# Kernel optimization log

Hardware: AMD Instinct MI355X
Metric: run time of the kernel (lower is better)

## Reference

```python
import jax, jax.numpy as jnp
import numpy as np

SIZES = (20, 20, 20, 20, 20)          # formula_oh_sizes
OH_N = sum(SIZES)                      # 100
NUM_BINS = 65536                       # spect_bin.get_num_bins()
EPS_SIZE = 1e-4                        # eps added to subset size
IN_EPS = 1e-5                          # torch InstanceNorm1d default eps


def thermometer_oh(counts):
    # StructuredOneHot with accum=True: per-element thermometer encoding.
    # counts: (N, E) element counts -> (N, sum(SIZES)) with out[j]=1 iff j < count.
    outs = [(jnp.arange(s, dtype=counts.dtype)[None, :] < counts[:, i:i + 1]).astype(jnp.float32)
            for i, s in enumerate(SIZES)]
    return jnp.concatenate(outs, axis=-1)


def inorm(x):
    # InstanceNorm1d (affine=False) as applied here: normalize over last dim per row.
    m = jnp.mean(x, axis=-1, keepdims=True)
    v = jnp.var(x, axis=-1, keepdims=True)
    return (x - m) * jax.lax.rsqrt(v + IN_EPS)


def _lin(key, fan_in, fan_out):
    k1, k2 = jax.random.split(key)
    bound = 1.0 / np.sqrt(fan_in)
    W = jax.random.uniform(k1, (fan_in, fan_out), jnp.float32, -bound, bound)
    b = jax.random.uniform(k2, (fan_out,), jnp.float32, -bound, bound)
    return W, b


def setup_inputs():
    key = jax.random.key(0)
    ks = jax.random.split(key, 12)
    B, A, GF, S, P, E, D = 8, 48, 256, 4096, 32, 5, 256
    vert_feat_in = jax.random.normal(ks[0], (B, A, GF), jnp.float32)
    vert_mask_in = jnp.ones((B, A), jnp.float32)
    elem_idx = jax.random.randint(ks[1], (B, A), 0, E)
    vert_element_oh = jax.nn.one_hot(elem_idx, E, dtype=jnp.float32)
    adj_oh = jnp.zeros((B, A, A), jnp.float32)                      # unused by forward path
    atom_subsets = jax.random.randint(ks[2], (B, S, A), 0, 2).astype(jnp.int32)
    atom_subsets_peaks = jnp.zeros((1,), jnp.float32)               # unused (mass_idx/intensity used)
    mass_idx = jax.random.randint(ks[3], (B, S, P), 0, NUM_BINS).astype(jnp.int32)
    intensity = jax.random.uniform(ks[4], (B, S, P), jnp.float32)
    combine_W, combine_b = _lin(ks[5], OH_N + GF, GF)
    l1_W, l1_b = _lin(ks[6], GF, D)
    l2a_W, l2a_b = _lin(ks[7], D, D)
    l2b_W, l2b_b = _lin(ks[8], D, D)
    score_W, score_b = _lin(ks[9], D, 1)
    return {
        'vert_feat_in': vert_feat_in, 'vert_mask_in': vert_mask_in,
        'vert_element_oh': vert_element_oh, 'adj_oh': adj_oh,
        'atom_subsets': atom_subsets, 'atom_subsets_peaks': atom_subsets_peaks,
        'mass_idx': mass_idx, 'intensity': intensity,
        'combine_W': combine_W, 'combine_b': combine_b,
        'l1_W': l1_W, 'l1_b': l1_b, 'l2a_W': l2a_W, 'l2a_b': l2a_b,
        'l2b_W': l2b_W, 'l2b_b': l2b_b, 'score_W': score_W, 'score_b': score_b,
    }


def reference(vert_feat_in, vert_mask_in, vert_element_oh, adj_oh, atom_subsets,
              atom_subsets_peaks, mass_idx, intensity,
              combine_W, combine_b, l1_W, l1_b, l2a_W, l2a_b, l2b_W, l2b_b,
              score_W, score_b):
    B, A, GF = vert_feat_in.shape
    _, S, _ = atom_subsets.shape
    subsets_f = atom_subsets.astype(jnp.float32)
    masked_vert = vert_feat_in * vert_mask_in[:, :, None]               # (B,A,GF)
    subsets_masked = subsets_f * vert_mask_in[:, None, :]               # (B,S,A)
    # weighted sum of vertex features over each subset
    sws = jnp.einsum('bag,bsa->bsg', masked_vert, subsets_masked)        # (B,S,GF)
    # per-subset element counts -> structured one-hot formula encoding
    counts = jnp.einsum('bae,bsa->bse', vert_element_oh, subsets_f)      # (B,S,E)
    pf_oh = thermometer_oh(counts.reshape(-1, counts.shape[-1])).reshape(B, S, OH_N)
    subset_size = jnp.sum(subsets_masked, axis=2) + EPS_SIZE             # (B,S)
    mean_feat = sws / subset_size[:, :, None]
    normed = inorm(mean_feat)                                            # subset_weighted_norm
    combined = jax.nn.relu(jnp.concatenate([pf_oh, normed], -1) @ combine_W + combine_b)
    x = inorm(combined)                                                  # norm_post_combine
    x = jax.nn.relu(x @ l1_W + l1_b)
    x = jax.nn.leaky_relu(x @ l2a_W + l2a_b)
    x = jax.nn.leaky_relu(x @ l2b_W + l2b_b)
    x = jax.nn.relu(x)
    x = inorm(x)                                                         # norm_pre_score
    scores = (x @ score_W + score_b)[..., 0]                             # (B,S)
    probs = jax.nn.softmax(scores, axis=-1)
    # per-batch sparse mass-matrix binning: scatter-add intensity*prob into spectral bins
    weighted = intensity * probs[:, :, None]                             # (B,S,P)
    seg = jax.vmap(lambda idx, w: jax.ops.segment_sum(w, idx, num_segments=NUM_BINS))
    spect_out = seg(mass_idx.reshape(B, -1), weighted.reshape(B, -1))    # (B,NUM_BINS)
    return spect_out, probs
```

## Files before the change

kernel.cpp:

```cpp
#include <hip/hip_runtime.h>
#include <math.h>

#define B_DIM 8
#define A_DIM 48
#define GF_DIM 256
#define S_DIM 4096
#define P_DIM 32
#define E_DIM 5
#define OHN 100
#define NBINS 65536

typedef __attribute__((ext_vector_type(8))) short short8v;
typedef __attribute__((ext_vector_type(4))) float float4v;

__device__ __forceinline__ float wave_sum(float v) {
#pragma unroll
    for (int o = 32; o; o >>= 1) v += __shfl_xor(v, o, 64);
    return v;
}
__device__ __forceinline__ float wave_max(float v) {
#pragma unroll
    for (int o = 32; o; o >>= 1) v = fmaxf(v, __shfl_xor(v, o, 64));
    return v;
}
__device__ __forceinline__ float quad16_sum(float v) {
    v += __shfl_xor(v, 1, 64); v += __shfl_xor(v, 2, 64);
    v += __shfl_xor(v, 4, 64); v += __shfl_xor(v, 8, 64);
    return v;
}
__device__ __forceinline__ unsigned short bf16_rn(float x) {
    unsigned int u = __float_as_uint(x);
    return (unsigned short)((u + 0x7FFFu + ((u >> 16) & 1u)) >> 16);
}
__device__ __forceinline__ float bf16_val(unsigned short h) {
    return __uint_as_float(((unsigned int)h) << 16);
}

__global__ __launch_bounds__(256) void k_wprep(
    const float* __restrict__ cW, const float* __restrict__ l1W,
    const float* __restrict__ l2aW, const float* __restrict__ l2bW,
    short* __restrict__ wp)
{
    int e = blockIdx.x * 256 + threadIdx.x;
    int c = e >> 13;
    int i = e & 8191;
    int j    = i & 7;
    int lane = (i >> 3) & 63;
    int nt   = (i >> 9) & 1;
    int wn   = i >> 10;
    int krel = (lane >> 4) * 8 + j;
    int n    = wn * 32 + nt * 16 + (lane & 15);
    float val = 0.f;
    if (c < 12) {
        int kp = c * 32 + krel;
        if (kp < 100)       val = cW[kp * 256 + n];
        else if (kp >= 128) val = cW[(kp - 28) * 256 + n];
    } else {
        int L  = (c - 12) >> 3;
        int kc = (c - 12) & 7;
        const float* W = (L == 0) ? l1W : (L == 1) ? l2aW : l2bW;
        val = W[(kc * 32 + krel) * 256 + n];
    }
    unsigned short h = bf16_rn(val);
    float lo = val - bf16_val(h);
    int base = c * 16384 + (i & 511);
    wp[base + (wn * 4 + nt) * 512]     = (short)h;
    wp[base + (wn * 4 + 2 + nt) * 512] = (short)bf16_rn(lo);
}

#define OFF_XF   49152
#define OFF_XAL  115712
#define OFF_PS   148480
#define OFF_CNT  150528
#define OFF_MASK 151808
#define OFF_EI   152000

__device__ __forceinline__ float4v mfma_bf16(short8v a, short8v b, float4v c) {
    return __builtin_amdgcn_mfma_f32_16x16x32_bf16(a, b, c, 0, 0, 0);
}

template <int NKC, int LO0, int ACT, bool NORM, bool SCORE>
__device__ __forceinline__ void layer_pass(
    short* xAh, short* xAl, float (*ps)[64],
    const short* __restrict__ wstream, const float* __restrict__ bias,
    const float* __restrict__ sW, const float* __restrict__ sb,
    float* __restrict__ scores, int R0)
{
    const int tid  = threadIdx.x;
    const int lane = tid & 63;
    const int wn   = tid >> 6;
    const int quad = lane >> 4;
    const int col  = lane & 15;
    const short* wbase = wstream + wn * 2048 + lane * 8;

    float4v acc[4][2];
#pragma unroll
    for (int mi = 0; mi < 4; ++mi)
#pragma unroll
        for (int nt = 0; nt < 2; ++nt) acc[mi][nt] = (float4v){0.f, 0.f, 0.f, 0.f};

    short8v bh[2][2], bl[2][2];
    bh[0][0] = *(const short8v*)(wbase);
    bh[0][1] = *(const short8v*)(wbase + 512);
    bl[0][0] = *(const short8v*)(wbase + 1024);
    bl[0][1] = *(const short8v*)(wbase + 1536);

#pragma unroll
    for (int kc = 0; kc < NKC; ++kc) {
        const int cur = kc & 1;
        if (kc + 1 < NKC) {
            const short* p = wbase + (kc + 1) * 16384;
            bh[cur ^ 1][0] = *(const short8v*)(p);
            bh[cur ^ 1][1] = *(const short8v*)(p + 512);
            bl[cur ^ 1][0] = *(const short8v*)(p + 1024);
            bl[cur ^ 1][1] = *(const short8v*)(p + 1536);
        }
        short8v ah[4], al[4];
#pragma unroll
        for (int mi = 0; mi < 4; ++mi)
            ah[mi] = *(const short8v*)(xAh + ((kc * 4 + mi) * 64 + lane) * 8);
        const bool hlo = (kc >= LO0);
        if (hlo) {
#pragma unroll
            for (int mi = 0; mi < 4; ++mi)
                al[mi] = *(const short8v*)(xAl + (((kc - LO0) * 4 + mi) * 64 + lane) * 8);
        }
#pragma unroll
        for (int mi = 0; mi < 4; ++mi)
#pragma unroll
            for (int nt = 0; nt < 2; ++nt) {
                acc[mi][nt] = mfma_bf16(ah[mi], bh[cur][nt], acc[mi][nt]);
                acc[mi][nt] = mfma_bf16(ah[mi], bl[cur][nt], acc[mi][nt]);
                if (hlo)
                    acc[mi][nt] = mfma_bf16(al[mi], bh[cur][nt], acc[mi][nt]);
            }
    }

    float bc0 = bias[wn * 32 + col];
    float bc1 = bias[wn * 32 + 16 + col];
#pragma unroll
    for (int mi = 0; mi < 4; ++mi)
#pragma unroll
        for (int r = 0; r < 4; ++r) {
            float z0 = acc[mi][0][r] + bc0;
            float z1 = acc[mi][1][r] + bc1;
            if (ACT == 0) { z0 = fmaxf(z0, 0.f); z1 = fmaxf(z1, 0.f); }
            else { z0 = (z0 > 0.f) ? z0 : 0.01f * z0; z1 = (z1 > 0.f) ? z1 : 0.01f * z1; }
            acc[mi][0][r] = z0; acc[mi][1][r] = z1;
        }

    __syncthreads();

    if (NORM) {
        float rsum[4][4];
#pragma unroll
        for (int mi = 0; mi < 4; ++mi)
#pragma unroll
            for (int r = 0; r < 4; ++r)
                rsum[mi][r] = quad16_sum(acc[mi][0][r] + acc[mi][1][r]);
        if (col == 0) {
#pragma unroll
            for (int mi = 0; mi < 4; ++mi)
#pragma unroll
                for (int r = 0; r < 4; ++r)
                    ps[wn][mi * 16 + quad * 4 + r] = rsum[mi][r];
        }
        __syncthreads();
        float mu[4][4];
#pragma unroll
        for (int mi = 0; mi < 4; ++mi)
#pragma unroll
            for (int r = 0; r < 4; ++r) {
                int m = mi * 16 + quad * 4 + r;
                float s = 0.f;
#pragma unroll
                for (int w = 0; w < 8; ++w) s += ps[w][m];
                mu[mi][r] = s * (1.f / 256.f);
            }
        __syncthreads();
        float qs[4][4];
#pragma unroll
        for (int mi = 0; mi < 4; ++mi)
#pragma unroll
            for (int r = 0; r < 4; ++r) {
                acc[mi][0][r] -= mu[mi][r];
                acc[mi][1][r] -= mu[mi][r];
                float q = acc[mi][0][r] * acc[mi][0][r]
                        + acc[mi][1][r] * acc[mi][1][r];
                qs[mi][r] = quad16_sum(q);
            }
        if (col == 0) {
#pragma unroll
            for (int mi = 0; mi < 4; ++mi)
#pragma unroll
                for (int r = 0; r < 4; ++r)
                    ps[wn][mi * 16 + quad * 4 + r] = qs[mi][r];
        }
        __syncthreads();
#pragma unroll
        for (int mi = 0; mi < 4; ++mi)
#pragma unroll
            for (int r = 0; r < 4; ++r) {
                int m = mi * 16 + quad * 4 + r;
                float s = 0.f;
#pragma unroll
                for (int w = 0; w < 8; ++w) s += ps[w][m];
                float rsf = 1.0f / sqrtf(s * (1.f / 256.f) + 1e-5f);
                acc[mi][0][r] *= rsf;
                acc[mi][1][r] *= rsf;
            }
    }

    if (SCORE) {
        __syncthreads();
        float sv0 = sW[wn * 32 + col];
        float sv1 = sW[wn * 32 + 16 + col];
        float psu[4][4];
#pragma unroll
        for (int mi = 0; mi < 4; ++mi)
#pragma unroll
            for (int r = 0; r < 4; ++r)
                psu[mi][r] = quad16_sum(acc[mi][0][r] * sv0 + acc[mi][1][r] * sv1);
        if (col == 0) {
#pragma unroll
            for (int mi = 0; mi < 4; ++mi)
#pragma unroll
                for (int r = 0; r < 4; ++r)
                    ps[wn][mi * 16 + quad * 4 + r] = psu[mi][r];
        }
        __syncthreads();
        if (tid < 64) {
            float s = sb[0];
#pragma unroll
            for (int w = 0; w < 8; ++w) s += ps[w][tid];
            scores[R0 + tid] = s;
        }
    } else {
#pragma unroll
        for (int mi = 0; mi < 4; ++mi)
#pragma unroll
            for (int nt = 0; nt < 2; ++nt) {
                int nn0 = (wn * 32 + nt * 16 + col) & ~1;
                int q2  = (nn0 & 31) >> 3;
                int j0  = nn0 & 7;
#pragma unroll
                for (int r = 0; r < 4; ++r) {
                    float v  = acc[mi][nt][r];
                    float pv = __shfl_xor(v, 1, 64);
                    int m15 = quad * 4 + r;
                    int rowidx = (wn * 4 + mi) * 64 + q2 * 16 + m15;
                    if ((col & 1) == 0) {
                        unsigned int wd = (unsigned int)bf16_rn(v)
                                        | ((unsigned int)bf16_rn(pv) << 16);
                        ((unsigned int*)xAh)[rowidx * 4 + (j0 >> 1)] = wd;
                    } else {
                        float ls = v  - bf16_val(bf16_rn(v));
                        float lp = pv - bf16_val(bf16_rn(pv));
                        unsigned int wd = (unsigned int)bf16_rn(lp)
                                        | ((unsigned int)bf16_rn(ls) << 16);
                        ((unsigned int*)xAl)[rowidx * 4 + (j0 >> 1)] = wd;
                    }
                }
            }
        __syncthreads();
    }
}

__global__ __launch_bounds__(512, 2) void k_mega(
    const float* __restrict__ vert_feat, const float* __restrict__ vert_mask,
    const float* __restrict__ elem_oh, const int* __restrict__ subsets,
    const short* __restrict__ wprep,
    const float* __restrict__ cb,  const float* __restrict__ l1b,
    const float* __restrict__ l2ab, const float* __restrict__ l2bb,
    const float* __restrict__ sW,  const float* __restrict__ sb,
    float* __restrict__ scores)
{
    __shared__ __align__(16) char smem[152192];
    short*  xAh   = (short*)smem;
    float*  xf    = (float*)(smem + OFF_XF);
    short*  xAl   = (short*)(smem + OFF_XAL);
    float (*ps)[64] = (float(*)[64])(smem + OFF_PS);
    float (*cnt)[5] = (float(*)[5])(smem + OFF_CNT);
    float*  maskL = (float*)(smem + OFF_MASK);
    int*    eiL   = (int*)(smem + OFF_EI);
    float4* vertm = (float4*)smem;

    const int tid  = threadIdx.x;
    const int lane = tid & 63;
    const int wn   = tid >> 6;
    const int fb   = blockIdx.x;
    const int b    = fb >> 6;
    const int R0   = fb * 64;

    if (tid < A_DIM) {
        maskL[tid] = vert_mask[b * A_DIM + tid];
        int ei = 0;
#pragma unroll
        for (int e = 0; e < E_DIM; ++e)
            if (elem_oh[(b * A_DIM + tid) * E_DIM + e] > 0.5f) ei = e;
        eiL[tid] = ei;
    }
    __syncthreads();

    {
        const float4* vb = (const float4*)(vert_feat + (size_t)b * A_DIM * GF_DIM);
        for (int idx = tid; idx < A_DIM * 64; idx += 512) {
            float4 v = vb[idx];
            float mk = maskL[idx >> 6];
            v.x *= mk; v.y *= mk; v.z *= mk; v.w *= mk;
            vertm[idx] = v;
        }
    }
    __syncthreads();

    {
        const float mymask = (lane < A_DIM) ? maskL[lane] : 0.f;
        const int   myei   = (lane < A_DIM) ? eiL[lane]   : -1;
#pragma unroll
        for (int i = 0; i < 8; ++i) {
            const int r = wn * 8 + i;
            const int* fp = subsets + ((size_t)fb * 64 + r) * A_DIM;
            int myflag = (lane < A_DIM) ? fp[lane] : 0;
            float fcoef = (float)myflag * mymask;

            float c0, c1, c2, c3, c4;
            {
                unsigned long long m0 = __ballot(myflag != 0 && myei == 0);
                unsigned long long m1 = __ballot(myflag != 0 && myei == 1);
                unsigned long long m2 = __ballot(myflag != 0 && myei == 2);
                unsigned long long m3 = __ballot(myflag != 0 && myei == 3);
                unsigned long long m4 = __ballot(myflag != 0 && myei == 4);
                c0 = (float)__popcll(m0); c1 = (float)__popcll(m1);
                c2 = (float)__popcll(m2); c3 = (float)__popcll(m3);
                c4 = (float)__popcll(m4);
            }
            float ssize = wave_sum(fcoef) + 1e-4f;

            float4 acc = make_float4(0.f, 0.f, 0.f, 0.f);
            for (int a = 0; a < A_DIM; ++a) {
                float cf = __shfl(fcoef, a, 64);
                float4 vv = vertm[a * 64 + lane];
                acc.x = fmaf(cf, vv.x, acc.x);
                acc.y = fmaf(cf, vv.y, acc.y);
                acc.z = fmaf(cf, vv.z, acc.z);
                acc.w = fmaf(cf, vv.w, acc.w);
            }
            float inv = 1.0f / ssize;
            float4 mv = make_float4(acc.x * inv, acc.y * inv,
                                    acc.z * inv, acc.w * inv);
            float t = wave_sum(mv.x + mv.y + mv.z + mv.w);
            float m = t * (1.0f / 256.0f);
            float dx = mv.x - m, dy = mv.y - m, dz = mv.z - m, dw = mv.w - m;
            float q = wave_sum(dx * dx + dy * dy + dz * dz + dw * dw);
            float rs = 1.0f / sqrtf(q * (1.0f / 256.0f) + 1e-5f);

            *(float4*)(xf + r * 260 + lane * 4) =
                make_float4(dx * rs, dy * rs, dz * rs, dw * rs);
            if (lane == 0) {
                cnt[r][0] = c0; cnt[r][1] = c1; cnt[r][2] = c2;
                cnt[r][3] = c3; cnt[r][4] = c4;
            }
        }
    }
    __syncthreads();

    {
#pragma unroll
        for (int g0 = 0; g0 < 6; ++g0) {
            int g  = tid + g0 * 512;
            int lt = g & 63;
            int t2 = g >> 6;
            int kc = t2 >> 2, mi = t2 & 3;
            int m  = mi * 16 + (lt & 15);
            int kb = (lt >> 4) * 8;
            if (kc < 4) {
                short8v hv;
#pragma unroll
                for (int j = 0; j < 8; ++j) {
                    int kp = kc * 32 + kb + j;
                    float val = 0.f;
                    if (kp < 100) {
                        int e = kp / 20;
                        val = ((float)(kp - e * 20) < cnt[m][e]) ? 1.0f : 0.0f;
                    }
                    hv[j] = (short)bf16_rn(val);
                }
                *(short8v*)(xAh + g * 8) = hv;
            } else {
                const float* src = xf + m * 260 + (kc - 4) * 32 + kb;
                float4 f0 = *(const float4*)(src);
                float4 f1 = *(const float4*)(src + 4);
                float fv[8] = {f0.x, f0.y, f0.z, f0.w, f1.x, f1.y, f1.z, f1.w};
                short8v hv, lv;
#pragma unroll
                for (int j = 0; j < 8; ++j) {
                    unsigned short h = bf16_rn(fv[j]);
                    hv[j] = (short)h;
                    lv[j] = (short)bf16_rn(fv[j] - bf16_val(h));
                }
                *(short8v*)(xAh + g * 8) = hv;
                *(short8v*)(xAl + (g - 1024) * 8) = lv;
            }
        }
    }
    __syncthreads();

    layer_pass<12, 4, 0, true,  false>(xAh, xAl, ps, wprep,
        cb, nullptr, nullptr, nullptr, R0);
    layer_pass< 8, 0, 0, false, false>(xAh, xAl, ps, wprep + 12 * 16384,
        l1b, nullptr, nullptr, nullptr, R0);
    layer_pass< 8, 0, 1, false, false>(xAh, xAl, ps, wprep + 20 * 16384,
        l2ab, nullptr, nullptr, nullptr, R0);
    layer_pass< 8, 0, 0, true,  true >(xAh, xAl, ps, wprep + 28 * 16384,
        l2bb, sW, sb, scores, R0);
}

__global__ __launch_bounds__(256) void k_softmax(float* __restrict__ probs) {
    const int b   = blockIdx.x;
    const int tid = threadIdx.x;
    __shared__ float redA[4];
    __shared__ float redB[4];
    float* sp = probs + (size_t)b * S_DIM;

    float v[16];
    float mx = -INFINITY;
#pragma unroll
    for (int i = 0; i < 16; ++i) {
        v[i] = sp[tid + i * 256];
        mx = fmaxf(mx, v[i]);
    }
    mx = wave_max(mx);
    if ((tid & 63) == 0) redA[tid >> 6] = mx;
    __syncthreads();
    mx = fmaxf(fmaxf(redA[0], redA[1]), fmaxf(redA[2], redA[3]));

    float sum = 0.f;
#pragma unroll
    for (int i = 0; i < 16; ++i) {
        v[i] = expf(v[i] - mx);
        sum += v[i];
    }
    sum = wave_sum(sum);
    if ((tid & 63) == 0) redB[tid >> 6] = sum;
    __syncthreads();
    float tot = redB[0] + redB[1] + redB[2] + redB[3];
    float inv = 1.0f / tot;
#pragma unroll
    for (int i = 0; i < 16; ++i) sp[tid + i * 256] = v[i] * inv;
}

__global__ __launch_bounds__(256) void k_zero(float* __restrict__ p, int n) {
    int i = blockIdx.x * 256 + threadIdx.x;
    if (i < n) p[i] = 0.0f;
}

__global__ __launch_bounds__(256) void k_scatter(
    const int*   __restrict__ mass_idx,
    const float* __restrict__ intensity,
    const float* __restrict__ probs,
    float* __restrict__ spect)
{
    int i  = blockIdx.x * 256 + threadIdx.x;
    int bs = i >> 5;
    int b  = i >> 17;
    float w = intensity[i] * probs[bs];
    unsafeAtomicAdd(spect + ((size_t)b << 16) + mass_idx[i], w);
}

extern "C" void kernel_launch(void* const* d_in, const int* in_sizes, int n_in,
                              void* d_out, int out_size, void* d_ws, size_t ws_size,
                              hipStream_t stream) {
    const float* vert_feat = (const float*)d_in[0];
    const float* vert_mask = (const float*)d_in[1];
    const float* elem_oh   = (const float*)d_in[2];
    const int*   subsets   = (const int*)d_in[4];
    const int*   mass_idx  = (const int*)d_in[6];
    const float* intensity = (const float*)d_in[7];
    const float* combine_W = (const float*)d_in[8];
    const float* combine_b = (const float*)d_in[9];
    const float* l1_W      = (const float*)d_in[10];
    const float* l1_b      = (const float*)d_in[11];
    const float* l2a_W     = (const float*)d_in[12];
    const float* l2a_b     = (const float*)d_in[13];
    const float* l2b_W     = (const float*)d_in[14];
    const float* l2b_b     = (const float*)d_in[15];
    const float* score_W   = (const float*)d_in[16];
    const float* score_b   = (const float*)d_in[17];

    float* out   = (float*)d_out;
    float* spect = out;
    float* probs = out + (size_t)B_DIM * NBINS;
    short* wprep = (short*)d_ws;

    k_wprep<<<1152, 256, 0, stream>>>(combine_W, l1_W, l2a_W, l2b_W, wprep);
    k_mega<<<512, 512, 0, stream>>>(vert_feat, vert_mask, elem_oh, subsets,
        wprep, combine_b, l1_b, l2a_b, l2b_b, score_W, score_b, probs);
    k_softmax<<<B_DIM, 256, 0, stream>>>(probs);
    k_zero<<<(B_DIM * NBINS) / 256, 256, 0, stream>>>(spect, B_DIM * NBINS);
    k_scatter<<<(B_DIM * S_DIM * P_DIM) / 256, 256, 0, stream>>>(
        mass_idx, intensity, probs, spect);
}
```

Baseline: 286.1 us.

## Split feature pooling into separate kernel and halve MLP tile rows

The fused mega-kernel is split in two. A new feature kernel computes the masked subset mean, its instance norm and the element counts, and writes them to a workspace buffer. The MLP kernel then runs on 32-row tiles with half the LDS footprint and two blocks' worth of extra occupancy (launch bounds 4), and its weight prefetch goes from double to triple buffering. The zero-fill kernel is also vectorised to float4. In exchange, the intermediate features make an extra round trip through global memory, and each weight chunk is re-read by twice as many blocks.

```diff
diff --git a/kernel.cpp b/kernel.cpp
--- a/kernel.cpp
+++ b/kernel.cpp
@@ -9,6 +9,7 @@
 #define E_DIM 5
 #define OHN 100
 #define NBINS 65536
+#define XF_STRIDE 268
 
 typedef __attribute__((ext_vector_type(8))) short short8v;
 typedef __attribute__((ext_vector_type(4))) float float4v;
@@ -68,12 +69,92 @@
     wp[base + (wn * 4 + 2 + nt) * 512] = (short)bf16_rn(lo);
 }
 
-#define OFF_XF   49152
-#define OFF_XAL  115712
-#define OFF_PS   148480
-#define OFF_CNT  150528
-#define OFF_MASK 151808
-#define OFF_EI   152000
+__global__ __launch_bounds__(256) void k_features(
+    const float* __restrict__ vert_feat, const float* __restrict__ vert_mask,
+    const float* __restrict__ elem_oh, const int* __restrict__ subsets,
+    float* __restrict__ x0)
+{
+    __shared__ float4 vertm[A_DIM][GF_DIM / 4];
+    __shared__ float  maskL[A_DIM];
+    __shared__ int    eiL[A_DIM];
+
+    const int tid  = threadIdx.x;
+    const int lane = tid & 63;
+    const int w    = tid >> 6;
+    const int b    = blockIdx.x >> 9;
+    const int s0   = (blockIdx.x & 511) * 8;
+
+    if (tid < A_DIM) {
+        maskL[tid] = vert_mask[b * A_DIM + tid];
+        int ei = 0;
+#pragma unroll
+        for (int e = 0; e < E_DIM; ++e)
+            if (elem_oh[(b * A_DIM + tid) * E_DIM + e] > 0.5f) ei = e;
+        eiL[tid] = ei;
+    }
+    __syncthreads();
+
+    const float4* vb = (const float4*)(vert_feat + (size_t)b * A_DIM * GF_DIM);
+    for (int idx = tid; idx < A_DIM * (GF_DIM / 4); idx += 256) {
+        float4 v = vb[idx];
+        float mk = maskL[idx >> 6];
+        v.x *= mk; v.y *= mk; v.z *= mk; v.w *= mk;
+        vertm[idx >> 6][idx & 63] = v;
+    }
+    __syncthreads();
+
+    const int   myei   = (lane < A_DIM) ? eiL[lane] : -1;
+    const float mymask = (lane < A_DIM) ? maskL[lane] : 0.0f;
+
+#pragma unroll
+    for (int i = 0; i < 2; ++i) {
+        const int s = s0 + w * 2 + i;
+        const int* fp = subsets + ((size_t)b * S_DIM + s) * A_DIM;
+        int myflag = (lane < A_DIM) ? fp[lane] : 0;
+        float fcoef = (float)myflag * mymask;
+
+        float c0, c1, c2, c3, c4;
+        {
+            unsigned long long m0 = __ballot(myflag != 0 && myei == 0);
+            unsigned long long m1 = __ballot(myflag != 0 && myei == 1);
+            unsigned long long m2 = __ballot(myflag != 0 && myei == 2);
+            unsigned long long m3 = __ballot(myflag != 0 && myei == 3);
+            unsigned long long m4 = __ballot(myflag != 0 && myei == 4);
+            c0 = (float)__popcll(m0); c1 = (float)__popcll(m1);
+            c2 = (float)__popcll(m2); c3 = (float)__popcll(m3);
+            c4 = (float)__popcll(m4);
+        }
+        float ssize = wave_sum(fcoef) + 1e-4f;
+
+        float4 acc = make_float4(0.f, 0.f, 0.f, 0.f);
+        for (int a = 0; a < A_DIM; ++a) {
+            float cf = __shfl(fcoef, a, 64);
+            float4 vv = vertm[a][lane];
+            acc.x = fmaf(cf, vv.x, acc.x);
+            acc.y = fmaf(cf, vv.y, acc.y);
+            acc.z = fmaf(cf, vv.z, acc.z);
+            acc.w = fmaf(cf, vv.w, acc.w);
+        }
+        float inv = 1.0f / ssize;
+        float4 mv = make_float4(acc.x * inv, acc.y * inv, acc.z * inv, acc.w * inv);
+
+        float t = wave_sum(mv.x + mv.y + mv.z + mv.w);
+        float m = t * (1.0f / 256.0f);
+        float dx = mv.x - m, dy = mv.y - m, dz = mv.z - m, dw = mv.w - m;
+        float q = wave_sum(dx * dx + dy * dy + dz * dz + dw * dw);
+        float rs = 1.0f / sqrtf(q * (1.0f / 256.0f) + 1e-5f);
+
+        float* xr = x0 + (size_t)(b * S_DIM + s) * XF_STRIDE;
+        *(float4*)(xr + lane * 4) = make_float4(dx * rs, dy * rs, dz * rs, dw * rs);
+        if (lane < E_DIM)
+            xr[256 + lane] = (lane == 0) ? c0 : (lane == 1) ? c1
+                           : (lane == 2) ? c2 : (lane == 3) ? c3 : c4;
+    }
+}
+
+#define OFF_XF  24576
+#define OFF_XAL 58880
+#define OFF_PS  75264
 
 __device__ __forceinline__ float4v mfma_bf16(short8v a, short8v b, float4v c) {
     return __builtin_amdgcn_mfma_f32_16x16x32_bf16(a, b, c, 0, 0, 0);
@@ -81,7 +162,7 @@
 
 template <int NKC, int LO0, int ACT, bool NORM, bool SCORE>
 __device__ __forceinline__ void layer_pass(
-    short* xAh, short* xAl, float (*ps)[64],
+    short* xAh, short* xAl, float (*ps)[32],
     const short* __restrict__ wstream, const float* __restrict__ bias,
     const float* __restrict__ sW, const float* __restrict__ sb,
     float* __restrict__ scores, int R0)
@@ -93,40 +174,47 @@
     const int col  = lane & 15;
     const short* wbase = wstream + wn * 2048 + lane * 8;
 
-    float4v acc[4][2];
-#pragma unroll
-    for (int mi = 0; mi < 4; ++mi)
+    float4v acc[2][2];
+#pragma unroll
+    for (int mi = 0; mi < 2; ++mi)
 #pragma unroll
         for (int nt = 0; nt < 2; ++nt) acc[mi][nt] = (float4v){0.f, 0.f, 0.f, 0.f};
 
-    short8v bh[2][2], bl[2][2];
-    bh[0][0] = *(const short8v*)(wbase);
-    bh[0][1] = *(const short8v*)(wbase + 512);
-    bl[0][0] = *(const short8v*)(wbase + 1024);
-    bl[0][1] = *(const short8v*)(wbase + 1536);
+    short8v bh[3][2], bl[3][2];
+#pragma unroll
+    for (int p = 0; p < 2; ++p) {
+        if (p < NKC) {
+            const short* q = wbase + p * 16384;
+            bh[p][0] = *(const short8v*)(q);
+            bh[p][1] = *(const short8v*)(q + 512);
+            bl[p][0] = *(const short8v*)(q + 1024);
+            bl[p][1] = *(const short8v*)(q + 1536);
+        }
+    }
 
 #pragma unroll
     for (int kc = 0; kc < NKC; ++kc) {
-        const int cur = kc & 1;
-        if (kc + 1 < NKC) {
-            const short* p = wbase + (kc + 1) * 16384;
-            bh[cur ^ 1][0] = *(const short8v*)(p);
-            bh[cur ^ 1][1] = *(const short8v*)(p + 512);
-            bl[cur ^ 1][0] = *(const short8v*)(p + 1024);
-            bl[cur ^ 1][1] = *(const short8v*)(p + 1536);
-        }
-        short8v ah[4], al[4];
-#pragma unroll
-        for (int mi = 0; mi < 4; ++mi)
-            ah[mi] = *(const short8v*)(xAh + ((kc * 4 + mi) * 64 + lane) * 8);
+        const int cur = kc % 3;
+        if (kc + 2 < NKC) {
+            const int nxt = (kc + 2) % 3;
+            const short* q = wbase + (kc + 2) * 16384;
+            bh[nxt][0] = *(const short8v*)(q);
+            bh[nxt][1] = *(const short8v*)(q + 512);
+            bl[nxt][0] = *(const short8v*)(q + 1024);
+            bl[nxt][1] = *(const short8v*)(q + 1536);
+        }
+        short8v ah[2], al[2];
+#pragma unroll
+        for (int mi = 0; mi < 2; ++mi)
+            ah[mi] = *(const short8v*)(xAh + ((kc * 2 + mi) * 64 + lane) * 8);
         const bool hlo = (kc >= LO0);
         if (hlo) {
 #pragma unroll
-            for (int mi = 0; mi < 4; ++mi)
-                al[mi] = *(const short8v*)(xAl + (((kc - LO0) * 4 + mi) * 64 + lane) * 8);
-        }
-#pragma unroll
-        for (int mi = 0; mi < 4; ++mi)
+            for (int mi = 0; mi < 2; ++mi)
+                al[mi] = *(const short8v*)(xAl + (((kc - LO0) * 2 + mi) * 64 + lane) * 8);
+        }
+#pragma unroll
+        for (int mi = 0; mi < 2; ++mi)
 #pragma unroll
             for (int nt = 0; nt < 2; ++nt) {
                 acc[mi][nt] = mfma_bf16(ah[mi], bh[cur][nt], acc[mi][nt]);
@@ -139,7 +227,7 @@
     float bc0 = bias[wn * 32 + col];
     float bc1 = bias[wn * 32 + 16 + col];
 #pragma unroll
-    for (int mi = 0; mi < 4; ++mi)
+    for (int mi = 0; mi < 2; ++mi)
 #pragma unroll
         for (int r = 0; r < 4; ++r) {
             float z0 = acc[mi][0][r] + bc0;
@@ -152,23 +240,23 @@
     __syncthreads();
 
     if (NORM) {
-        float rsum[4][4];
-#pragma unroll
-        for (int mi = 0; mi < 4; ++mi)
+        float rsum[2][4];
+#pragma unroll
+        for (int mi = 0; mi < 2; ++mi)
 #pragma unroll
             for (int r = 0; r < 4; ++r)
                 rsum[mi][r] = quad16_sum(acc[mi][0][r] + acc[mi][1][r]);
         if (col == 0) {
 #pragma unroll
-            for (int mi = 0; mi < 4; ++mi)
+            for (int mi = 0; mi < 2; ++mi)
 #pragma unroll
                 for (int r = 0; r < 4; ++r)
                     ps[wn][mi * 16 + quad * 4 + r] = rsum[mi][r];
         }
         __syncthreads();
-        float mu[4][4];
-#pragma unroll
-        for (int mi = 0; mi < 4; ++mi)
+        float mu[2][4];
+#pragma unroll
+        for (int mi = 0; mi < 2; ++mi)
 #pragma unroll
             for (int r = 0; r < 4; ++r) {
                 int m = mi * 16 + quad * 4 + r;
@@ -178,9 +266,9 @@
                 mu[mi][r] = s * (1.f / 256.f);
             }
         __syncthreads();
-        float qs[4][4];
-#pragma unroll
-        for (int mi = 0; mi < 4; ++mi)
+        float qs[2][4];
+#pragma unroll
+        for (int mi = 0; mi < 2; ++mi)
 #pragma unroll
             for (int r = 0; r < 4; ++r) {
                 acc[mi][0][r] -= mu[mi][r];
@@ -191,14 +279,14 @@
             }
         if (col == 0) {
 #pragma unroll
-            for (int mi = 0; mi < 4; ++mi)
+            for (int mi = 0; mi < 2; ++mi)
 #pragma unroll
                 for (int r = 0; r < 4; ++r)
                     ps[wn][mi * 16 + quad * 4 + r] = qs[mi][r];
         }
         __syncthreads();
 #pragma unroll
-        for (int mi = 0; mi < 4; ++mi)
+        for (int mi = 0; mi < 2; ++mi)
 #pragma unroll
             for (int r = 0; r < 4; ++r) {
                 int m = mi * 16 + quad * 4 + r;
@@ -215,21 +303,21 @@
         __syncthreads();
         float sv0 = sW[wn * 32 + col];
         float sv1 = sW[wn * 32 + 16 + col];
-        float psu[4][4];
-#pragma unroll
-        for (int mi = 0; mi < 4; ++mi)
+        float psu[2][4];
+#pragma unroll
+        for (int mi = 0; mi < 2; ++mi)
 #pragma unroll
             for (int r = 0; r < 4; ++r)
                 psu[mi][r] = quad16_sum(acc[mi][0][r] * sv0 + acc[mi][1][r] * sv1);
         if (col == 0) {
 #pragma unroll
-            for (int mi = 0; mi < 4; ++mi)
+            for (int mi = 0; mi < 2; ++mi)
 #pragma unroll
                 for (int r = 0; r < 4; ++r)
                     ps[wn][mi * 16 + quad * 4 + r] = psu[mi][r];
         }
         __syncthreads();
-        if (tid < 64) {
+        if (tid < 32) {
             float s = sb[0];
 #pragma unroll
             for (int w = 0; w < 8; ++w) s += ps[w][tid];
@@ -237,18 +325,18 @@
         }
     } else {
 #pragma unroll
-        for (int mi = 0; mi < 4; ++mi)
+        for (int mi = 0; mi < 2; ++mi)
 #pragma unroll
             for (int nt = 0; nt < 2; ++nt) {
-                int nn0 = (wn * 32 + nt * 16 + col) & ~1;
-                int q2  = (nn0 & 31) >> 3;
+                int nn0 = (nt * 16 + col) & ~1;
+                int q2  = nn0 >> 3;
                 int j0  = nn0 & 7;
 #pragma unroll
                 for (int r = 0; r < 4; ++r) {
                     float v  = acc[mi][nt][r];
                     float pv = __shfl_xor(v, 1, 64);
                     int m15 = quad * 4 + r;
-                    int rowidx = (wn * 4 + mi) * 64 + q2 * 16 + m15;
+                    int rowidx = (wn * 2 + mi) * 64 + q2 * 16 + m15;
                     if ((col & 1) == 0) {
                         unsigned int wd = (unsigned int)bf16_rn(v)
                                         | ((unsigned int)bf16_rn(pv) << 16);
@@ -266,114 +354,42 @@
     }
 }
 
-__global__ __launch_bounds__(512, 2) void k_mega(
-    const float* __restrict__ vert_feat, const float* __restrict__ vert_mask,
-    const float* __restrict__ elem_oh, const int* __restrict__ subsets,
-    const short* __restrict__ wprep,
+__global__ __launch_bounds__(512, 4) void k_mlp(
+    const float* __restrict__ x0, const short* __restrict__ wprep,
     const float* __restrict__ cb,  const float* __restrict__ l1b,
     const float* __restrict__ l2ab, const float* __restrict__ l2bb,
     const float* __restrict__ sW,  const float* __restrict__ sb,
     float* __restrict__ scores)
 {
-    __shared__ __align__(16) char smem[152192];
-    short*  xAh   = (short*)smem;
-    float*  xf    = (float*)(smem + OFF_XF);
-    short*  xAl   = (short*)(smem + OFF_XAL);
-    float (*ps)[64] = (float(*)[64])(smem + OFF_PS);
-    float (*cnt)[5] = (float(*)[5])(smem + OFF_CNT);
-    float*  maskL = (float*)(smem + OFF_MASK);
-    int*    eiL   = (int*)(smem + OFF_EI);
-    float4* vertm = (float4*)smem;
-
-    const int tid  = threadIdx.x;
-    const int lane = tid & 63;
-    const int wn   = tid >> 6;
-    const int fb   = blockIdx.x;
-    const int b    = fb >> 6;
-    const int R0   = fb * 64;
-
-    if (tid < A_DIM) {
-        maskL[tid] = vert_mask[b * A_DIM + tid];
-        int ei = 0;
-#pragma unroll
-        for (int e = 0; e < E_DIM; ++e)
-            if (elem_oh[(b * A_DIM + tid) * E_DIM + e] > 0.5f) ei = e;
-        eiL[tid] = ei;
-    }
-    __syncthreads();
+    __shared__ __align__(16) char smem[76288];
+    short*  xAh = (short*)smem;
+    float*  xf  = (float*)(smem + OFF_XF);
+    short*  xAl = (short*)(smem + OFF_XAL);
+    float (*ps)[32] = (float(*)[32])(smem + OFF_PS);
+
+    const int tid = threadIdx.x;
+    const int fb  = blockIdx.x;
+    const int R0  = fb * 32;
 
     {
-        const float4* vb = (const float4*)(vert_feat + (size_t)b * A_DIM * GF_DIM);
-        for (int idx = tid; idx < A_DIM * 64; idx += 512) {
-            float4 v = vb[idx];
-            float mk = maskL[idx >> 6];
-            v.x *= mk; v.y *= mk; v.z *= mk; v.w *= mk;
-            vertm[idx] = v;
-        }
+        const float4* src = (const float4*)(x0 + (size_t)fb * 32 * XF_STRIDE);
+        for (int i = tid; i < 2144; i += 512) ((float4*)xf)[i] = src[i];
     }
     __syncthreads();
 
     {
-        const float mymask = (lane < A_DIM) ? maskL[lane] : 0.f;
-        const int   myei   = (lane < A_DIM) ? eiL[lane]   : -1;
-#pragma unroll
-        for (int i = 0; i < 8; ++i) {
-            const int r = wn * 8 + i;
-            const int* fp = subsets + ((size_t)fb * 64 + r) * A_DIM;
-            int myflag = (lane < A_DIM) ? fp[lane] : 0;
-            float fcoef = (float)myflag * mymask;
-
-            float c0, c1, c2, c3, c4;
-            {
-                unsigned long long m0 = __ballot(myflag != 0 && myei == 0);
-                unsigned long long m1 = __ballot(myflag != 0 && myei == 1);
-                unsigned long long m2 = __ballot(myflag != 0 && myei == 2);
-                unsigned long long m3 = __ballot(myflag != 0 && myei == 3);
-                unsigned long long m4 = __ballot(myflag != 0 && myei == 4);
-                c0 = (float)__popcll(m0); c1 = (float)__popcll(m1);
-                c2 = (float)__popcll(m2); c3 = (float)__popcll(m3);
-                c4 = (float)__popcll(m4);
-            }
-            float ssize = wave_sum(fcoef) + 1e-4f;
-
-            float4 acc = make_float4(0.f, 0.f, 0.f, 0.f);
-            for (int a = 0; a < A_DIM; ++a) {
-                float cf = __shfl(fcoef, a, 64);
-                float4 vv = vertm[a * 64 + lane];
-                acc.x = fmaf(cf, vv.x, acc.x);
-                acc.y = fmaf(cf, vv.y, acc.y);
-                acc.z = fmaf(cf, vv.z, acc.z);
-                acc.w = fmaf(cf, vv.w, acc.w);
-            }
-            float inv = 1.0f / ssize;
-            float4 mv = make_float4(acc.x * inv, acc.y * inv,
-                                    acc.z * inv, acc.w * inv);
-            float t = wave_sum(mv.x + mv.y + mv.z + mv.w);
-            float m = t * (1.0f / 256.0f);
-            float dx = mv.x - m, dy = mv.y - m, dz = mv.z - m, dw = mv.w - m;
-            float q = wave_sum(dx * dx + dy * dy + dz * dz + dw * dw);
-            float rs = 1.0f / sqrtf(q * (1.0f / 256.0f) + 1e-5f);
-
-            *(float4*)(xf + r * 260 + lane * 4) =
-                make_float4(dx * rs, dy * rs, dz * rs, dw * rs);
-            if (lane == 0) {
-                cnt[r][0] = c0; cnt[r][1] = c1; cnt[r][2] = c2;
-                cnt[r][3] = c3; cnt[r][4] = c4;
-            }
-        }
-    }
-    __syncthreads();
-
-    {
-#pragma unroll
-        for (int g0 = 0; g0 < 6; ++g0) {
+#pragma unroll
+        for (int g0 = 0; g0 < 3; ++g0) {
             int g  = tid + g0 * 512;
             int lt = g & 63;
             int t2 = g >> 6;
-            int kc = t2 >> 2, mi = t2 & 3;
+            int kc = t2 >> 1, mi = t2 & 1;
             int m  = mi * 16 + (lt & 15);
             int kb = (lt >> 4) * 8;
             if (kc < 4) {
+                float c[5];
+#pragma unroll
+                for (int e = 0; e < 5; ++e) c[e] = xf[m * XF_STRIDE + 256 + e];
                 short8v hv;
 #pragma unroll
                 for (int j = 0; j < 8; ++j) {
@@ -381,15 +397,15 @@
                     float val = 0.f;
                     if (kp < 100) {
                         int e = kp / 20;
-                        val = ((float)(kp - e * 20) < cnt[m][e]) ? 1.0f : 0.0f;
+                        val = ((float)(kp - e * 20) < c[e]) ? 1.0f : 0.0f;
                     }
                     hv[j] = (short)bf16_rn(val);
                 }
                 *(short8v*)(xAh + g * 8) = hv;
             } else {
-                const float* src = xf + m * 260 + (kc - 4) * 32 + kb;
-                float4 f0 = *(const float4*)(src);
-                float4 f1 = *(const float4*)(src + 4);
+                const float* srcp = xf + m * XF_STRIDE + (kc - 4) * 32 + kb;
+                float4 f0 = *(const float4*)(srcp);
+                float4 f1 = *(const float4*)(srcp + 4);
                 float fv[8] = {f0.x, f0.y, f0.z, f0.w, f1.x, f1.y, f1.z, f1.w};
                 short8v hv, lv;
 #pragma unroll
@@ -399,7 +415,7 @@
                     lv[j] = (short)bf16_rn(fv[j] - bf16_val(h));
                 }
                 *(short8v*)(xAh + g * 8) = hv;
-                *(short8v*)(xAl + (g - 1024) * 8) = lv;
+                *(short8v*)(xAl + (g - 512) * 8) = lv;
             }
         }
     }
@@ -449,9 +465,9 @@
     for (int i = 0; i < 16; ++i) sp[tid + i * 256] = v[i] * inv;
 }
 
-__global__ __launch_bounds__(256) void k_zero(float* __restrict__ p, int n) {
+__global__ __launch_bounds__(256) void k_zero4(float4* __restrict__ p, int n4) {
     int i = blockIdx.x * 256 + threadIdx.x;
-    if (i < n) p[i] = 0.0f;
+    if (i < n4) p[i] = make_float4(0.f, 0.f, 0.f, 0.f);
 }
 
 __global__ __launch_bounds__(256) void k_scatter(
@@ -490,13 +506,17 @@
     float* out   = (float*)d_out;
     float* spect = out;
     float* probs = out + (size_t)B_DIM * NBINS;
+
     short* wprep = (short*)d_ws;
+    float* x0    = (float*)(wprep + 36 * 16384);
 
     k_wprep<<<1152, 256, 0, stream>>>(combine_W, l1_W, l2a_W, l2b_W, wprep);
-    k_mega<<<512, 512, 0, stream>>>(vert_feat, vert_mask, elem_oh, subsets,
-        wprep, combine_b, l1_b, l2a_b, l2b_b, score_W, score_b, probs);
+    k_features<<<4096, 256, 0, stream>>>(vert_feat, vert_mask, elem_oh, subsets, x0);
+    k_mlp<<<1024, 512, 0, stream>>>(x0, wprep,
+        combine_b, l1_b, l2a_b, l2b_b, score_W, score_b, probs);
     k_softmax<<<B_DIM, 256, 0, stream>>>(probs);
-    k_zero<<<(B_DIM * NBINS) / 256, 256, 0, stream>>>(spect, B_DIM * NBINS);
+    k_zero4<<<(B_DIM * NBINS / 4) / 256, 256, 0, stream>>>(
+        (float4*)spect, B_DIM * NBINS / 4);
     k_scatter<<<(B_DIM * S_DIM * P_DIM) / 256, 256, 0, stream>>>(
         mass_idx, intensity, probs, spect);
 }
```

Result: no change. 284.6 us (-0.5%).
